# Kernel tuning notes

Measured on AMD Instinct MI355X. Metric: run time of the kernel, lower is better.

## Reference

```python
import jax, jax.numpy as jnp
import numpy as np

N = 20000   # nodes
E = 640000  # edges (avg degree 32)
D = 128     # input_nf == output_nf
H = 128     # hidden_size


def silu(x):
    return x * jax.nn.sigmoid(x)


def setup_inputs() -> dict:
    key = jax.random.key(0)
    ks = jax.random.split(key, 16)
    def lin(k, out_d, in_d, scale=None):
        s = scale if scale is not None else (1.0 / np.sqrt(in_d))
        return jax.random.uniform(k, (out_d, in_d), jnp.float32, -s, s)
    return {
        "h": jax.random.normal(ks[0], (N, D), jnp.float32),
        "coord": jax.random.normal(ks[1], (N, 3), jnp.float32),
        "edge_index": jax.random.randint(ks[2], (2, E), 0, N, jnp.int32),
        # edge_mlp: Linear(2D+1 -> H), Linear(H -> H)
        "We1": lin(ks[3], H, 2 * D + 1), "be1": jnp.zeros((H,), jnp.float32),
        "We2": lin(ks[4], H, H),          "be2": jnp.zeros((H,), jnp.float32),
        # node_mlp: Linear(H+D -> H), Linear(H -> D)
        "Wn1": lin(ks[5], H, H + D),      "bn1": jnp.zeros((H,), jnp.float32),
        "Wn2": lin(ks[6], D, H),          "bn2": jnp.zeros((D,), jnp.float32),
        # coord_mlp: Linear(H -> H), Linear(H -> 1, no bias, xavier gain=0.001)
        "Wc1": lin(ks[7], H, H),          "bc1": jnp.zeros((H,), jnp.float32),
        "Wc2": lin(ks[8], 1, H, scale=0.001 * np.sqrt(6.0 / (H + 1))),
    }


def reference(h, coord, edge_index, We1, be1, We2, be2, Wn1, bn1, Wn2, bn2, Wc1, bc1, Wc2):
    src, dst = edge_index[0], edge_index[1]

    # coord2radial (normalize=False)
    coord_diff = coord[src] - coord[dst]                 # [E, 3]
    radial = jnp.sum(coord_diff * coord_diff, axis=1, keepdims=True)  # [E, 1]

    # edge model: cat(h[src], h[dst], radial) -> Lin -> SiLU -> Lin -> SiLU
    e_in = jnp.concatenate([h[src], h[dst], radial], axis=1)  # [E, 2D+1]
    edge_feat = silu(silu(e_in @ We1.T + be1) @ We2.T + be2)  # [E, H]

    # coord model: coord_diff * coord_mlp(edge_feat), scatter-add over src
    w = silu(edge_feat @ Wc1.T + bc1) @ Wc2.T                 # [E, 1]
    trans = coord_diff * w                                    # [E, 3]
    coord_out = coord + jax.ops.segment_sum(trans, src, num_segments=N)

    # node model: agg edge_feat over src, cat(h, agg) -> Lin -> SiLU -> Lin, residual
    agg = jax.ops.segment_sum(edge_feat, src, num_segments=N)  # [N, H]
    n_in = jnp.concatenate([h, agg], axis=1)                   # [N, H+D]
    h_out = h + (silu(n_in @ Wn1.T + bn1) @ Wn2.T + bn2)       # [N, D]

    return (h_out, coord_out)
```

## Files before the change

### kernel.cpp

```cpp
#include <hip/hip_runtime.h>

#define N_NODES 20000
#define N_EDGES 640000
#define D 128
#define H 128

#define EB    128
#define TPB   512
#define NBLK2 512
#define NTILE (N_EDGES / EB)
#define EBN   64
#define NNT64 ((N_NODES + EBN - 1) / EBN)
#define ST    136

#define WS_W1   0
#define WS_W2   65536
#define WS_WC1  98304
#define WS_WN1  131072
#define WS_WN2  196608
#define WS_CNT  229376
#define WS_CUR  309376
#define WS_PERM 389376
#define WS_U    2949376
#define WS_V    8069376
#define WS_P    13189376

typedef short bf16x8 __attribute__((ext_vector_type(8)));
typedef float f32x4  __attribute__((ext_vector_type(4)));

__device__ __forceinline__ float silu_f(float x) {
    return x * __builtin_amdgcn_rcpf(1.0f + __expf(-x));
}
__device__ __forceinline__ ushort f2b(float f) {
    union { float f; unsigned int u; } v; v.f = f;
    return (ushort)((v.u + 0x7FFF + ((v.u >> 16) & 1)) >> 16);
}
__device__ __forceinline__ float b2f(ushort s) {
    union { unsigned int u; float f; } v; v.u = ((unsigned int)s) << 16; return v.f;
}

__device__ __forceinline__ void gemm_chunk_rw(const ushort* Ab, int kc0,
                                              const bf16x8 b[2], f32x4 acc[4][2],
                                              int eg, int lane)
{
    const int r = lane & 15, g = lane >> 4;
    bf16x8 a[4];
    #pragma unroll
    for (int mt = 0; mt < 4; ++mt)
        a[mt] = *(const bf16x8*)&Ab[(eg * 64 + mt * 16 + r) * ST + kc0 + g * 8];
    #pragma unroll
    for (int mt = 0; mt < 4; ++mt)
        #pragma unroll
        for (int nt = 0; nt < 2; ++nt)
            acc[mt][nt] = __builtin_amdgcn_mfma_f32_16x16x32_bf16(a[mt], b[nt], acc[mt][nt], 0, 0, 0);
}

__device__ __forceinline__ void zero_acc8(f32x4 acc[4][2]) {
    #pragma unroll
    for (int mt = 0; mt < 4; ++mt)
        #pragma unroll
        for (int nt = 0; nt < 2; ++nt)
            acc[mt][nt] = (f32x4){0.f, 0.f, 0.f, 0.f};
}

__device__ __forceinline__ void epi_silu8(f32x4 acc[4][2], const float* bias,
                                          ushort* out, int eg, int cg, int lane) {
    const int r = lane & 15, g = lane >> 4;
    #pragma unroll
    for (int nt = 0; nt < 2; ++nt) {
        int o = cg * 32 + nt * 16 + r;
        float bo = bias[o];
        #pragma unroll
        for (int mt = 0; mt < 4; ++mt)
            #pragma unroll
            for (int j = 0; j < 4; ++j) {
                int e = eg * 64 + mt * 16 + g * 4 + j;
                out[e * ST + o] = f2b(silu_f(acc[mt][nt][j] + bo));
            }
    }
}

__global__ void prep2(const float* __restrict__ We1, const float* __restrict__ We2,
                      const float* __restrict__ Wc1, const float* __restrict__ Wn1,
                      const float* __restrict__ Wn2, const float* __restrict__ coordp,
                      const int* __restrict__ eidx,
                      ushort* w1, ushort* w2, ushort* wc1, ushort* wn1, ushort* wn2,
                      float* cout, int* cnt)
{
    int idx = blockIdx.x * 256 + threadIdx.x;
    if (idx < N_EDGES) atomicAdd(&cnt[eidx[idx]], 1);
    int j = idx;
    if (j < 32768) { w1[j] = f2b(We1[(j >> 8) * 257 + (j & 255)]); return; }
    j -= 32768;
    if (j < 16384) { w2[j] = f2b(We2[j]); return; }
    j -= 16384;
    if (j < 16384) { wc1[j] = f2b(Wc1[j]); return; }
    j -= 16384;
    if (j < 32768) { wn1[j] = f2b(Wn1[j]); return; }
    j -= 32768;
    if (j < 16384) { wn2[j] = f2b(Wn2[j]); return; }
    j -= 16384;
    if (j < N_NODES * 3) cout[j] = coordp[j];
}

__global__ __launch_bounds__(256, 2)
void uvp_k(const float* __restrict__ h,
           const ushort* __restrict__ w1b, const ushort* __restrict__ wn1b,
           const float* __restrict__ be1, const float* __restrict__ bn1,
           ushort* __restrict__ u, ushort* __restrict__ v, ushort* __restrict__ p)
{
    __shared__ __align__(16) ushort hs[EBN * ST];
    __shared__ float b1s[H], bn1s[H];

    const int tid = threadIdx.x, lane = tid & 63, wv = tid >> 6;
    const int eg = wv >> 2, cg = wv & 3;
    const int r = lane & 15, g = lane >> 4;
    const int n0 = blockIdx.x * EBN;

    if (tid < 128) b1s[tid] = be1[tid];
    else if (tid < 256) bn1s[tid - 128] = bn1[tid - 128];

    bf16x8 wa[4][2], wb[4][2], wn[4][2];
    {
        const int c0 = cg * 32 + r, c1c = c0 + 16;
        #pragma unroll
        for (int kc = 0; kc < 4; ++kc) {
            wa[kc][0] = *(const bf16x8*)&w1b [c0  * 256 +       kc * 32 + g * 8];
            wa[kc][1] = *(const bf16x8*)&w1b [c1c * 256 +       kc * 32 + g * 8];
            wb[kc][0] = *(const bf16x8*)&w1b [c0  * 256 + 128 + kc * 32 + g * 8];
            wb[kc][1] = *(const bf16x8*)&w1b [c1c * 256 + 128 + kc * 32 + g * 8];
            wn[kc][0] = *(const bf16x8*)&wn1b[c0  * 256 +       kc * 32 + g * 8];
            wn[kc][1] = *(const bf16x8*)&wn1b[c1c * 256 +       kc * 32 + g * 8];
        }
    }
    #pragma unroll
    for (int it = 0; it < 8; ++it) {
        int idx = tid + it * 256;
        int e = idx >> 5, c = idx & 31;
        int n = n0 + e; if (n >= N_NODES) n = 0;
        float4 vv = *(const float4*)&h[(size_t)n * D + c * 4];
        ushort4 pk; pk.x = f2b(vv.x); pk.y = f2b(vv.y); pk.z = f2b(vv.z); pk.w = f2b(vv.w);
        *(ushort4*)&hs[e * ST + c * 4] = pk;
    }
    __syncthreads();

    f32x4 acc[4][2];
    zero_acc8(acc);
    #pragma unroll
    for (int kc = 0; kc < 4; ++kc) gemm_chunk_rw(hs, kc * 32, wa[kc], acc, eg, lane);
    #pragma unroll
    for (int nt = 0; nt < 2; ++nt) {
        int o = cg * 32 + nt * 16 + r;
        float bo = b1s[o];
        #pragma unroll
        for (int mt = 0; mt < 4; ++mt)
            #pragma unroll
            for (int j = 0; j < 4; ++j) {
                int n = n0 + eg * 64 + mt * 16 + g * 4 + j;
                if (n < N_NODES) u[(size_t)n * H + o] = f2b(acc[mt][nt][j] + bo);
            }
    }
    zero_acc8(acc);
    #pragma unroll
    for (int kc = 0; kc < 4; ++kc) gemm_chunk_rw(hs, kc * 32, wb[kc], acc, eg, lane);
    #pragma unroll
    for (int nt = 0; nt < 2; ++nt) {
        int o = cg * 32 + nt * 16 + r;
        #pragma unroll
        for (int mt = 0; mt < 4; ++mt)
            #pragma unroll
            for (int j = 0; j < 4; ++j) {
                int n = n0 + eg * 64 + mt * 16 + g * 4 + j;
                if (n < N_NODES) v[(size_t)n * H + o] = f2b(acc[mt][nt][j]);
            }
    }
    zero_acc8(acc);
    #pragma unroll
    for (int kc = 0; kc < 4; ++kc) gemm_chunk_rw(hs, kc * 32, wn[kc], acc, eg, lane);
    #pragma unroll
    for (int nt = 0; nt < 2; ++nt) {
        int o = cg * 32 + nt * 16 + r;
        float bo = bn1s[o];
        #pragma unroll
        for (int mt = 0; mt < 4; ++mt)
            #pragma unroll
            for (int j = 0; j < 4; ++j) {
                int n = n0 + eg * 64 + mt * 16 + g * 4 + j;
                if (n < N_NODES) p[(size_t)n * H + o] = f2b(acc[mt][nt][j] + bo);
            }
    }
}

__global__ void scan_k(const int* __restrict__ cnt, int* cur) {
    __shared__ int wsum[16];
    __shared__ int carry_s;
    const int t = threadIdx.x, lane = t & 63, wid = t >> 6;
    if (t == 0) carry_s = 0;
    __syncthreads();
    for (int base = 0; base < N_NODES; base += 1024) {
        int i = base + t;
        int vv = (i < N_NODES) ? cnt[i] : 0;
        int s = vv;
        #pragma unroll
        for (int d = 1; d < 64; d <<= 1) {
            int x = __shfl_up(s, d);
            if (lane >= d) s += x;
        }
        if (lane == 63) wsum[wid] = s;
        __syncthreads();
        if (wid == 0) {
            int ws = (lane < 16) ? wsum[lane] : 0;
            #pragma unroll
            for (int d = 1; d < 16; d <<= 1) {
                int x = __shfl_up(ws, d);
                if (lane >= d) ws += x;
            }
            if (lane < 16) wsum[lane] = ws;
        }
        __syncthreads();
        int woff = (wid > 0) ? wsum[wid - 1] : 0;
        if (i < N_NODES) cur[i] = carry_s + woff + s - vv;
        __syncthreads();
        if (t == 0) carry_s += wsum[15];
        __syncthreads();
    }
}

__global__ void scatter_k(const int* __restrict__ eidx, int* cur, int* perm) {
    int e = blockIdx.x * 256 + threadIdx.x;
    if (e < N_EDGES) {
        int pp = atomicAdd(&cur[eidx[e]], 1);
        perm[pp] = e;
    }
}

__global__ __launch_bounds__(TPB, 4)
void egcl_edge(const ushort* __restrict__ u, const ushort* __restrict__ v,
               const int* __restrict__ eidx, const int* __restrict__ perm,
               const float* __restrict__ coordp,
               const ushort* __restrict__ w2b, const ushort* __restrict__ wc1b,
               const float* __restrict__ We1,
               const float* __restrict__ be2, const float* __restrict__ bc1,
               const float* __restrict__ Wc2,
               float* __restrict__ agg, float* __restrict__ coord_out)
{
    __shared__ __align__(16) ushort t1[EB * ST];
    __shared__ __align__(16) ushort ef[EB * ST];
    __shared__ int   srcs_s[2][EB], dsts_s[2][EB];
    __shared__ float radial_s[2][EB];
    __shared__ float cdx_s[2][EB], cdy_s[2][EB], cdz_s[2][EB];
    __shared__ float b2s[H], bc1s[H], wc2s[H], w256s[H];

    ushort* const c1 = t1;

    const int tid = threadIdx.x, lane = tid & 63, wv = tid >> 6;
    const int eg = wv >> 2, cg = wv & 3;
    const int r = lane & 15, g = lane >> 4;
    const int ce = tid >> 2, cq = tid & 3;

    if (tid < 128)      b2s[tid] = be2[tid];
    else if (tid < 256) bc1s[tid - 128] = bc1[tid - 128];
    else if (tid < 384) wc2s[tid - 256] = Wc2[tid - 256];
    else                w256s[tid - 384] = We1[(tid - 384) * 257 + 256];

    bf16x8 w2f[4][2], w3f[4][2];
    {
        const int c0 = cg * 32 + r, c1c = c0 + 16;
        #pragma unroll
        for (int kc = 0; kc < 4; ++kc) {
            w2f[kc][0] = *(const bf16x8*)&w2b [c0  * 128 + kc * 32 + g * 8];
            w2f[kc][1] = *(const bf16x8*)&w2b [c1c * 128 + kc * 32 + g * 8];
            w3f[kc][0] = *(const bf16x8*)&wc1b[c0  * 128 + kc * 32 + g * 8];
            w3f[kc][1] = *(const bf16x8*)&wc1b[c1c * 128 + kc * 32 + g * 8];
        }
    }

    const int tBeg = (int)(((long long)blockIdx.x * NTILE) / NBLK2);
    const int tEnd = (int)(((long long)(blockIdx.x + 1) * NTILE) / NBLK2);

    int rs = 0, rd = 0;
    float rsx = 0, rsy = 0, rsz = 0, rdx = 0, rdy = 0, rdz = 0;
    if (tid < EB) {
        int e = perm[tBeg * EB + tid];
        int s = eidx[e], d = eidx[N_EDGES + e];
        srcs_s[0][tid] = s; dsts_s[0][tid] = d;
        float sx = coordp[s * 3], sy = coordp[s * 3 + 1], sz = coordp[s * 3 + 2];
        float dx0 = coordp[d * 3], dy0 = coordp[d * 3 + 1], dz0 = coordp[d * 3 + 2];
        float dx = sx - dx0, dy = sy - dy0, dz = sz - dz0;
        cdx_s[0][tid] = dx; cdy_s[0][tid] = dy; cdz_s[0][tid] = dz;
        radial_s[0][tid] = dx * dx + dy * dy + dz * dz;
    }
    __syncthreads();

    bf16x8 uvr[8];
    {
        const ushort* up = u + (size_t)srcs_s[0][ce] * H + cq * 32;
        const ushort* vp = v + (size_t)dsts_s[0][ce] * H + cq * 32;
        #pragma unroll
        for (int i = 0; i < 4; ++i) {
            uvr[i]     = *(const bf16x8*)(up + i * 8);
            uvr[4 + i] = *(const bf16x8*)(vp + i * 8);
        }
    }
    if (tid < EB && tBeg + 1 < NTILE) {
        int e = perm[(tBeg + 1) * EB + tid];
        rs = eidx[e]; rd = eidx[N_EDGES + e];
        rsx = coordp[rs * 3]; rsy = coordp[rs * 3 + 1]; rsz = coordp[rs * 3 + 2];
        rdx = coordp[rd * 3]; rdy = coordp[rd * 3 + 1]; rdz = coordp[rd * 3 + 2];
    }

    f32x4 acc[4][2];
    int pb = 0;

    for (int t = tBeg; t < tEnd; ++t) {
        {
            float rad = radial_s[pb][ce];
            #pragma unroll
            for (int i = 0; i < 4; ++i) {
                float4 wlo = *(const float4*)&w256s[cq * 32 + i * 8];
                float4 whi = *(const float4*)&w256s[cq * 32 + i * 8 + 4];
                float wcol[8] = {wlo.x, wlo.y, wlo.z, wlo.w, whi.x, whi.y, whi.z, whi.w};
                bf16x8 uu = uvr[i], vx = uvr[4 + i];
                bf16x8 res;
                #pragma unroll
                for (int k = 0; k < 8; ++k) {
                    float x = b2f((ushort)uu[k]) + b2f((ushort)vx[k]) + rad * wcol[k];
                    res[k] = (short)f2b(silu_f(x));
                }
                *(bf16x8*)&t1[ce * ST + cq * 32 + i * 8] = res;
            }
        }
        if (tid < EB) {
            srcs_s[pb ^ 1][tid] = rs; dsts_s[pb ^ 1][tid] = rd;
            float dx = rsx - rdx, dy = rsy - rdy, dz = rsz - rdz;
            cdx_s[pb ^ 1][tid] = dx; cdy_s[pb ^ 1][tid] = dy; cdz_s[pb ^ 1][tid] = dz;
            radial_s[pb ^ 1][tid] = dx * dx + dy * dy + dz * dz;
        }
        __syncthreads();

        int en = 0;
        if (tid < EB && t + 2 < NTILE) en = perm[(t + 2) * EB + tid];
        zero_acc8(acc);
        __builtin_amdgcn_s_setprio(1);
        #pragma unroll
        for (int kc = 0; kc < 4; ++kc) gemm_chunk_rw(t1, kc * 32, w2f[kc], acc, eg, lane);
        __builtin_amdgcn_s_setprio(0);
        epi_silu8(acc, b2s, ef, eg, cg, lane);
        __syncthreads();

        int rs2 = 0, rd2 = 0;
        if (tid < EB) { rs2 = eidx[en]; rd2 = eidx[N_EDGES + en]; }
        zero_acc8(acc);
        __builtin_amdgcn_s_setprio(1);
        #pragma unroll
        for (int kc = 0; kc < 4; ++kc) gemm_chunk_rw(ef, kc * 32, w3f[kc], acc, eg, lane);
        __builtin_amdgcn_s_setprio(0);
        epi_silu8(acc, bc1s, c1, eg, cg, lane);
        {
            int o = tid & 127, q = tid >> 7;
            int base = q * 32;
            float sum = 0.f;
            int curs = srcs_s[pb][base];
            for (int k = 0; k < 32; ++k) {
                int e = base + k;
                int s = srcs_s[pb][e];
                if (s != curs) {
                    atomicAdd(&agg[(size_t)curs * D + o], sum);
                    sum = 0.f; curs = s;
                }
                sum += b2f(ef[e * ST + o]);
            }
            atomicAdd(&agg[(size_t)curs * D + o], sum);
        }
        __syncthreads();

        if (tid < EB) {
            rs = rs2; rd = rd2;
            rsx = coordp[rs * 3]; rsy = coordp[rs * 3 + 1]; rsz = coordp[rs * 3 + 2];
            rdx = coordp[rd * 3]; rdy = coordp[rd * 3 + 1]; rdz = coordp[rd * 3 + 2];
        }
        {
            const ushort* c1r = &c1[ce * ST + cq * 32];
            float s_ = 0.f;
            #pragma unroll
            for (int k = 0; k < 32; ++k) s_ += b2f(c1r[k]) * wc2s[cq * 32 + k];
            s_ += __shfl_down(s_, 2);
            s_ += __shfl_down(s_, 1);
            float wfull = __shfl(s_, lane & ~3);
            if (cq < 3) {
                float cdv = (cq == 0) ? cdx_s[pb][ce] : (cq == 1) ? cdy_s[pb][ce] : cdz_s[pb][ce];
                atomicAdd(&coord_out[(size_t)srcs_s[pb][ce] * 3 + cq], cdv * wfull);
            }
        }
        {
            const ushort* up = u + (size_t)srcs_s[pb ^ 1][ce] * H + cq * 32;
            const ushort* vp = v + (size_t)dsts_s[pb ^ 1][ce] * H + cq * 32;
            #pragma unroll
            for (int i = 0; i < 4; ++i) {
                uvr[i]     = *(const bf16x8*)(up + i * 8);
                uvr[4 + i] = *(const bf16x8*)(vp + i * 8);
            }
        }
        __syncthreads();
        pb ^= 1;
    }
}

__global__ __launch_bounds__(256, 4)
void egcl_node(const float* __restrict__ h,
               const ushort* __restrict__ wn1b, const ushort* __restrict__ wn2b,
               const ushort* __restrict__ pArr, const float* __restrict__ bn2,
               float* __restrict__ hout )
{
    __shared__ __align__(16) ushort t1[EBN * ST];
    __shared__ __align__(16) ushort t2[EBN * ST];
    __shared__ float b2s[H];

    const int tid = threadIdx.x, lane = tid & 63, wv = tid >> 6;
    const int eg = wv >> 2, cg = wv & 3;
    const int r = lane & 15, g = lane >> 4;
    const int n0 = blockIdx.x * EBN;

    if (tid < 128) b2s[tid] = bn2[tid];

    bf16x8 wnb[4][2], w2f[4][2];
    {
        const int c0 = cg * 32 + r, c1c = c0 + 16;
        #pragma unroll
        for (int kc = 0; kc < 4; ++kc) {
            wnb[kc][0] = *(const bf16x8*)&wn1b[c0  * 256 + 128 + kc * 32 + g * 8];
            wnb[kc][1] = *(const bf16x8*)&wn1b[c1c * 256 + 128 + kc * 32 + g * 8];
            w2f[kc][0] = *(const bf16x8*)&wn2b[c0  * 128 + kc * 32 + g * 8];
            w2f[kc][1] = *(const bf16x8*)&wn2b[c1c * 128 + kc * 32 + g * 8];
        }
    }
    #pragma unroll
    for (int it = 0; it < 8; ++it) {
        int idx = tid + it * 256;
        int e = idx >> 5, c = idx & 31;
        int n = n0 + e; if (n >= N_NODES) n = 0;
        float4 vv = *(const float4*)&hout[(size_t)n * D + c * 4];
        ushort4 pk; pk.x = f2b(vv.x); pk.y = f2b(vv.y); pk.z = f2b(vv.z); pk.w = f2b(vv.w);
        *(ushort4*)&t1[e * ST + c * 4] = pk;
    }
    __syncthreads();

    f32x4 acc[4][2];
    zero_acc8(acc);
    #pragma unroll
    for (int kc = 0; kc < 4; ++kc) gemm_chunk_rw(t1, kc * 32, wnb[kc], acc, eg, lane);
    #pragma unroll
    for (int nt = 0; nt < 2; ++nt) {
        int o = cg * 32 + nt * 16 + r;
        #pragma unroll
        for (int mt = 0; mt < 4; ++mt)
            #pragma unroll
            for (int j = 0; j < 4; ++j) {
                int e = eg * 64 + mt * 16 + g * 4 + j;
                int n = n0 + e; if (n >= N_NODES) n = 0;
                float x = acc[mt][nt][j] + b2f(pArr[(size_t)n * H + o]);
                t2[e * ST + o] = f2b(silu_f(x));
            }
    }
    __syncthreads();

    zero_acc8(acc);
    #pragma unroll
    for (int kc = 0; kc < 4; ++kc) gemm_chunk_rw(t2, kc * 32, w2f[kc], acc, eg, lane);
    #pragma unroll
    for (int nt = 0; nt < 2; ++nt) {
        int o = cg * 32 + nt * 16 + r;
        float bo = b2s[o];
        #pragma unroll
        for (int mt = 0; mt < 4; ++mt)
            #pragma unroll
            for (int j = 0; j < 4; ++j) {
                int n = n0 + eg * 64 + mt * 16 + g * 4 + j;
                if (n < N_NODES)
                    hout[(size_t)n * D + o] = h[(size_t)n * D + o] + acc[mt][nt][j] + bo;
            }
    }
}

extern "C" void kernel_launch(void* const* d_in, const int* in_sizes, int n_in,
                              void* d_out, int out_size, void* d_ws, size_t ws_size,
                              hipStream_t stream)
{
    const float* h     = (const float*)d_in[0];
    const float* coord = (const float*)d_in[1];
    const int*   eidx  = (const int*)d_in[2];
    const float* We1 = (const float*)d_in[3];
    const float* be1 = (const float*)d_in[4];
    const float* We2 = (const float*)d_in[5];
    const float* be2 = (const float*)d_in[6];
    const float* Wn1 = (const float*)d_in[7];
    const float* bn1 = (const float*)d_in[8];
    const float* Wn2 = (const float*)d_in[9];
    const float* bn2 = (const float*)d_in[10];
    const float* Wc1 = (const float*)d_in[11];
    const float* bc1 = (const float*)d_in[12];
    const float* Wc2 = (const float*)d_in[13];

    float* hout = (float*)d_out;
    float* cout = (float*)d_out + (size_t)N_NODES * D;

    char* ws = (char*)d_ws;
    ushort* w1b  = (ushort*)(ws + WS_W1);
    ushort* w2b  = (ushort*)(ws + WS_W2);
    ushort* wc1b = (ushort*)(ws + WS_WC1);
    ushort* wn1b = (ushort*)(ws + WS_WN1);
    ushort* wn2b = (ushort*)(ws + WS_WN2);
    int* cnt  = (int*)(ws + WS_CNT);
    int* cur  = (int*)(ws + WS_CUR);
    int* perm = (int*)(ws + WS_PERM);
    ushort* uArr = (ushort*)(ws + WS_U);
    ushort* vArr = (ushort*)(ws + WS_V);
    ushort* pArr = (ushort*)(ws + WS_P);

    hipMemsetAsync(hout, 0, (size_t)N_NODES * D * sizeof(float), stream);
    hipMemsetAsync(cnt, 0, N_NODES * sizeof(int), stream);
    prep2<<<(N_EDGES + 255) / 256, 256, 0, stream>>>(We1, We2, Wc1, Wn1, Wn2, coord, eidx,
                                                     w1b, w2b, wc1b, wn1b, wn2b, cout, cnt);
    scan_k<<<1, 1024, 0, stream>>>(cnt, cur);
    scatter_k<<<(N_EDGES + 255) / 256, 256, 0, stream>>>(eidx, cur, perm);
    uvp_k<<<NNT64, 256, 0, stream>>>(h, w1b, wn1b, be1, bn1, uArr, vArr, pArr);
    egcl_edge<<<NBLK2, TPB, 0, stream>>>(uArr, vArr, eidx, perm, coord,
                                         w2b, wc1b, We1, be2, bc1, Wc2,
                                         hout, cout);
    egcl_node<<<NNT64, 256, 0, stream>>>(h, wn1b, wn2b, pArr, bn2, hout);
}
```

Measured before the change: 342.6 us.

## Fuse coord MLP output projection into GEMM epilogue, pack bf16 conversions, interleave tiles

```diff
diff --git a/kernel.cpp b/kernel.cpp
--- a/kernel.cpp
+++ b/kernel.cpp
@@ -38,6 +38,11 @@
 __device__ __forceinline__ float b2f(ushort s) {
     union { unsigned int u; float f; } v; v.u = ((unsigned int)s) << 16; return v.f;
 }
+__device__ __forceinline__ unsigned f2b2(float lo, float hi) {
+    unsigned r;
+    asm("v_cvt_pk_bf16_f32 %0, %1, %2" : "=v"(r) : "v"(lo), "v"(hi));
+    return r;
+}
 
 __device__ __forceinline__ void gemm_chunk_rw(const ushort* Ab, int kc0,
                                               const bf16x8 b[2], f32x4 acc[4][2],
@@ -77,6 +82,26 @@
                 int e = eg * 64 + mt * 16 + g * 4 + j;
                 out[e * ST + o] = f2b(silu_f(acc[mt][nt][j] + bo));
             }
+    }
+}
+
+__device__ __forceinline__ void epi_silu8_pk(f32x4 acc[4][2], const float* bias,
+                                             ushort* out, int eg, int cg, int lane) {
+    const int r = lane & 15, g = lane >> 4;
+    #pragma unroll
+    for (int nt = 0; nt < 2; ++nt) {
+        int o = cg * 32 + nt * 16 + r;
+        float bo = bias[o];
+        #pragma unroll
+        for (int mt = 0; mt < 4; ++mt) {
+            int e = eg * 64 + mt * 16 + g * 4;
+            unsigned p01 = f2b2(silu_f(acc[mt][nt][0] + bo), silu_f(acc[mt][nt][1] + bo));
+            unsigned p23 = f2b2(silu_f(acc[mt][nt][2] + bo), silu_f(acc[mt][nt][3] + bo));
+            out[(e + 0) * ST + o] = (ushort)p01;
+            out[(e + 1) * ST + o] = (ushort)(p01 >> 16);
+            out[(e + 2) * ST + o] = (ushort)p23;
+            out[(e + 3) * ST + o] = (ushort)(p23 >> 16);
+        }
     }
 }
 
@@ -249,9 +274,8 @@
     __shared__ int   srcs_s[2][EB], dsts_s[2][EB];
     __shared__ float radial_s[2][EB];
     __shared__ float cdx_s[2][EB], cdy_s[2][EB], cdz_s[2][EB];
+    __shared__ float wcop[4][EB];
     __shared__ float b2s[H], bc1s[H], wc2s[H], w256s[H];
-
-    ushort* const c1 = t1;
 
     const int tid = threadIdx.x, lane = tid & 63, wv = tid >> 6;
     const int eg = wv >> 2, cg = wv & 3;
@@ -275,13 +299,11 @@
         }
     }
 
-    const int tBeg = (int)(((long long)blockIdx.x * NTILE) / NBLK2);
-    const int tEnd = (int)(((long long)(blockIdx.x + 1) * NTILE) / NBLK2);
-
+    int t = (int)blockIdx.x;
     int rs = 0, rd = 0;
     float rsx = 0, rsy = 0, rsz = 0, rdx = 0, rdy = 0, rdz = 0;
     if (tid < EB) {
-        int e = perm[tBeg * EB + tid];
+        int e = perm[t * EB + tid];
         int s = eidx[e], d = eidx[N_EDGES + e];
         srcs_s[0][tid] = s; dsts_s[0][tid] = d;
         float sx = coordp[s * 3], sy = coordp[s * 3 + 1], sz = coordp[s * 3 + 2];
@@ -302,8 +324,8 @@
             uvr[4 + i] = *(const bf16x8*)(vp + i * 8);
         }
     }
-    if (tid < EB && tBeg + 1 < NTILE) {
-        int e = perm[(tBeg + 1) * EB + tid];
+    if (tid < EB && t + NBLK2 < NTILE) {
+        int e = perm[(t + NBLK2) * EB + tid];
         rs = eidx[e]; rd = eidx[N_EDGES + e];
         rsx = coordp[rs * 3]; rsy = coordp[rs * 3 + 1]; rsz = coordp[rs * 3 + 2];
         rdx = coordp[rd * 3]; rdy = coordp[rd * 3 + 1]; rdz = coordp[rd * 3 + 2];
@@ -312,22 +334,26 @@
     f32x4 acc[4][2];
     int pb = 0;
 
-    for (int t = tBeg; t < tEnd; ++t) {
+    for (; t < NTILE; t += NBLK2) {
         {
             float rad = radial_s[pb][ce];
             #pragma unroll
             for (int i = 0; i < 4; ++i) {
                 float4 wlo = *(const float4*)&w256s[cq * 32 + i * 8];
                 float4 whi = *(const float4*)&w256s[cq * 32 + i * 8 + 4];
-                float wcol[8] = {wlo.x, wlo.y, wlo.z, wlo.w, whi.x, whi.y, whi.z, whi.w};
                 bf16x8 uu = uvr[i], vx = uvr[4 + i];
-                bf16x8 res;
-                #pragma unroll
-                for (int k = 0; k < 8; ++k) {
-                    float x = b2f((ushort)uu[k]) + b2f((ushort)vx[k]) + rad * wcol[k];
-                    res[k] = (short)f2b(silu_f(x));
-                }
-                *(bf16x8*)&t1[ce * ST + cq * 32 + i * 8] = res;
+                float x0 = silu_f(b2f((ushort)uu[0]) + b2f((ushort)vx[0]) + rad * wlo.x);
+                float x1 = silu_f(b2f((ushort)uu[1]) + b2f((ushort)vx[1]) + rad * wlo.y);
+                float x2 = silu_f(b2f((ushort)uu[2]) + b2f((ushort)vx[2]) + rad * wlo.z);
+                float x3 = silu_f(b2f((ushort)uu[3]) + b2f((ushort)vx[3]) + rad * wlo.w);
+                float x4 = silu_f(b2f((ushort)uu[4]) + b2f((ushort)vx[4]) + rad * whi.x);
+                float x5 = silu_f(b2f((ushort)uu[5]) + b2f((ushort)vx[5]) + rad * whi.y);
+                float x6 = silu_f(b2f((ushort)uu[6]) + b2f((ushort)vx[6]) + rad * whi.z);
+                float x7 = silu_f(b2f((ushort)uu[7]) + b2f((ushort)vx[7]) + rad * whi.w);
+                uint4 pk4;
+                pk4.x = f2b2(x0, x1); pk4.y = f2b2(x2, x3);
+                pk4.z = f2b2(x4, x5); pk4.w = f2b2(x6, x7);
+                *(uint4*)&t1[ce * ST + cq * 32 + i * 8] = pk4;
             }
         }
         if (tid < EB) {
@@ -339,23 +365,61 @@
         __syncthreads();
 
         int en = 0;
-        if (tid < EB && t + 2 < NTILE) en = perm[(t + 2) * EB + tid];
+        if (tid < EB && t + 2 * NBLK2 < NTILE) en = perm[(t + 2 * NBLK2) * EB + tid];
         zero_acc8(acc);
         __builtin_amdgcn_s_setprio(1);
         #pragma unroll
         for (int kc = 0; kc < 4; ++kc) gemm_chunk_rw(t1, kc * 32, w2f[kc], acc, eg, lane);
         __builtin_amdgcn_s_setprio(0);
-        epi_silu8(acc, b2s, ef, eg, cg, lane);
+        epi_silu8_pk(acc, b2s, ef, eg, cg, lane);
         __syncthreads();
 
         int rs2 = 0, rd2 = 0;
         if (tid < EB) { rs2 = eidx[en]; rd2 = eidx[N_EDGES + en]; }
-        zero_acc8(acc);
-        __builtin_amdgcn_s_setprio(1);
-        #pragma unroll
-        for (int kc = 0; kc < 4; ++kc) gemm_chunk_rw(ef, kc * 32, w3f[kc], acc, eg, lane);
-        __builtin_amdgcn_s_setprio(0);
-        epi_silu8(acc, bc1s, c1, eg, cg, lane);
+        {
+            f32x4 acc3[2][4];
+            #pragma unroll
+            for (int ot = 0; ot < 2; ++ot)
+                #pragma unroll
+                for (int et = 0; et < 4; ++et)
+                    acc3[ot][et] = (f32x4){0.f, 0.f, 0.f, 0.f};
+            __builtin_amdgcn_s_setprio(1);
+            #pragma unroll
+            for (int kc = 0; kc < 4; ++kc) {
+                bf16x8 bfr[4];
+                #pragma unroll
+                for (int et = 0; et < 4; ++et)
+                    bfr[et] = *(const bf16x8*)&ef[(eg * 64 + et * 16 + r) * ST + kc * 32 + g * 8];
+                #pragma unroll
+                for (int ot = 0; ot < 2; ++ot)
+                    #pragma unroll
+                    for (int et = 0; et < 4; ++et)
+                        acc3[ot][et] = __builtin_amdgcn_mfma_f32_16x16x32_bf16(
+                            w3f[kc][ot], bfr[et], acc3[ot][et], 0, 0, 0);
+            }
+            __builtin_amdgcn_s_setprio(0);
+            float partial[4] = {0.f, 0.f, 0.f, 0.f};
+            #pragma unroll
+            for (int ot = 0; ot < 2; ++ot) {
+                int ob = cg * 32 + ot * 16 + g * 4;
+                float4 wq = *(const float4*)&wc2s[ob];
+                float4 bq = *(const float4*)&bc1s[ob];
+                #pragma unroll
+                for (int et = 0; et < 4; ++et) {
+                    partial[et] += silu_f(acc3[ot][et][0] + bq.x) * wq.x
+                                 + silu_f(acc3[ot][et][1] + bq.y) * wq.y
+                                 + silu_f(acc3[ot][et][2] + bq.z) * wq.z
+                                 + silu_f(acc3[ot][et][3] + bq.w) * wq.w;
+                }
+            }
+            #pragma unroll
+            for (int et = 0; et < 4; ++et) {
+                float s_ = partial[et];
+                s_ += __shfl_xor(s_, 16);
+                s_ += __shfl_xor(s_, 32);
+                if (g == 0) wcop[cg][eg * 64 + et * 16 + r] = s_;
+            }
+        }
         {
             int o = tid & 127, q = tid >> 7;
             int base = q * 32;
@@ -380,10 +444,7 @@
             rdx = coordp[rd * 3]; rdy = coordp[rd * 3 + 1]; rdz = coordp[rd * 3 + 2];
         }
         {
-            const ushort* c1r = &c1[ce * ST + cq * 32];
-            float s_ = 0.f;
-            #pragma unroll
-            for (int k = 0; k < 32; ++k) s_ += b2f(c1r[k]) * wc2s[cq * 32 + k];
+            float s_ = wcop[cq][ce];
             s_ += __shfl_down(s_, 2);
             s_ += __shfl_down(s_, 1);
             float wfull = __shfl(s_, lane & ~3);
```

Measured after the change: 369.8 us. 7.9% more time.
